# Kernel optimization log

Measured on AMD Instinct MI355X. Metric: run time of the kernel, lower is better.

The kernel has to match this reference:

```python
import jax, jax.numpy as jnp
import numpy as np

EMBED = 1024
HEADS = 16
HEAD_DIM = EMBED // HEADS


def setup_inputs() -> dict:
    key = jax.random.key(0)
    ks = jax.random.split(key, 8)
    N, L = 2, 2048
    values = jax.random.normal(ks[0], (N, L, EMBED), dtype=jnp.float32)
    keys_ = jax.random.normal(ks[1], (N, L, EMBED), dtype=jnp.float32)
    query = jax.random.normal(ks[2], (N, L, EMBED), dtype=jnp.float32)
    mask = jnp.ones((N, 1, 1, L), dtype=jnp.int32)
    s = 1.0 / np.sqrt(EMBED)
    W_q = jax.random.normal(ks[3], (EMBED, EMBED), dtype=jnp.float32) * s
    W_k = jax.random.normal(ks[4], (EMBED, EMBED), dtype=jnp.float32) * s
    W_v = jax.random.normal(ks[5], (EMBED, EMBED), dtype=jnp.float32) * s
    W_o = jax.random.normal(ks[6], (EMBED, EMBED), dtype=jnp.float32) * s
    b_o = jax.random.normal(ks[7], (EMBED,), dtype=jnp.float32) * 0.01
    return {"values": values, "keys": keys_, "query": query, "mask": mask,
            "W_q": W_q, "W_k": W_k, "W_v": W_v, "W_o": W_o, "b_o": b_o}


def reference(values, keys, query, mask, W_q, W_k, W_v, W_o, b_o):
    N, Lq, _ = query.shape
    Lk = keys.shape[1]
    # projections (torch Linear: x @ W.T); reshape to (N, H, L, Dh)
    q = (query @ W_q.T).reshape(N, Lq, HEADS, HEAD_DIM).transpose(0, 2, 1, 3)
    k = (keys @ W_k.T).reshape(N, Lk, HEADS, HEAD_DIM).transpose(0, 2, 1, 3)
    v = (values @ W_v.T).reshape(N, Lk, HEADS, HEAD_DIM).transpose(0, 2, 1, 3)
    energy = jnp.einsum('bhqd,bhkd->bhqk', q, k) / jnp.sqrt(jnp.float32(HEAD_DIM))
    energy = jnp.where(mask == 0, jnp.float32(-1e20), energy)
    attn = jax.nn.softmax(energy, axis=-1)
    out = jnp.einsum('bhqk,bhkd->bhqd', attn, v)
    out = out.transpose(0, 2, 1, 3).reshape(N, Lq, EMBED)
    return out @ W_o.T + b_o
```

## Files before the change

### kernel.cpp

```cpp
#include <hip/hip_runtime.h>
#include <cstddef>
#include <cstdint>

#define SEQ    2048
#define NBATCH 2

typedef unsigned short u16;
typedef unsigned int   u32;
typedef __attribute__((ext_vector_type(8))) short bf16x8;
typedef __attribute__((ext_vector_type(4))) float f32x4;

#if __has_builtin(__builtin_amdgcn_exp2f)
#define EXP2F(x) __builtin_amdgcn_exp2f(x)
#else
#define EXP2F(x) exp2f(x)
#endif

#define GLL16(g, l) __builtin_amdgcn_global_load_lds( \
    (const __attribute__((address_space(1))) void*)(g), \
    (__attribute__((address_space(3))) void*)(l), 16, 0, 0)

__device__ __forceinline__ u32 fbits(float x) { union { float f; u32 u; } c; c.f = x; return c.u; }
__device__ __forceinline__ u16 f2bf(float x) { return (u16)((fbits(x) + 0x8000u) >> 16); }
__device__ __forceinline__ u32 pack2bf(float lo, float hi) {
    return __builtin_amdgcn_perm(fbits(hi) + 0x8000u, fbits(lo) + 0x8000u, 0x07060302u);
}

__global__ __launch_bounds__(256)
void cast_w(const float* __restrict__ wq, const float* __restrict__ wk,
            const float* __restrict__ wv, const float* __restrict__ wo,
            u16* __restrict__ owq, u16* __restrict__ owk,
            u16* __restrict__ owv, u16* __restrict__ owo)
{
    const int w = blockIdx.x >> 10, xi = blockIdx.x & 1023;
    const float* s; u16* d;
    if (w == 0)      { s = wq; d = owq; }
    else if (w == 1) { s = wk; d = owk; }
    else if (w == 2) { s = wv; d = owv; }
    else             { s = wo; d = owo; }
    const int i = xi * 256 + threadIdx.x;
    float4 vv = ((const float4*)s)[i];
    uint2 r; r.x = pack2bf(vv.x, vv.y); r.y = pack2bf(vv.z, vv.w);
    ((uint2*)d)[i] = r;
}

__device__ __forceinline__
void gemm_body_f32A(const float* __restrict__ X, const u16* __restrict__ W,
                    void* __restrict__ Yv, const int layout)
{
    __shared__ u16 smem[128 * 72 + 128 * 64];
    u16* As = smem;
    u16* Bs = smem + 128 * 72;

    const int tid  = threadIdx.x;
    const int wave = tid >> 6;
    const int lane = tid & 63;
    const int lm   = lane & 15;
    const int quad = lane >> 4;
    const int m0 = blockIdx.x * 128;
    const int n0 = blockIdx.y * 128;
    const int wr = (wave & 1) * 64;
    const int wc = (wave >> 1) * 64;

    const int srow = tid >> 1;
    const int scol = (tid & 1) * 32;
    const float* xg = X + (size_t)(m0 + srow) * 1024 + scol;
    const int brow = wave * 32 + (lane >> 3);
    const int bcol = (lane & 7) * 8;
    const u16* wg = W + (size_t)(n0 + brow) * 1024 + bcol;

    float4 pa[8];
    #pragma unroll
    for (int p = 0; p < 8; ++p) pa[p] = ((const float4*)xg)[p];

    f32x4 acc[4][4] = {};

    for (int k0 = 0; k0 < 1024; k0 += 64) {
        __syncthreads();
        #pragma unroll
        for (int p = 0; p < 4; ++p) {
            const float4 a = pa[2 * p], b = pa[2 * p + 1];
            union { u32 w[4]; bf16x8 v; } u;
            u.w[0] = pack2bf(a.x, a.y); u.w[1] = pack2bf(a.z, a.w);
            u.w[2] = pack2bf(b.x, b.y); u.w[3] = pack2bf(b.z, b.w);
            *(bf16x8*)&As[srow * 72 + scol + p * 8] = u.v;
            GLL16(wg + k0 + p * 8 * 1024, &Bs[(wave * 32 + p * 8) * 64]);
        }
        __syncthreads();
        if (k0 + 64 < 1024) {
            #pragma unroll
            for (int p = 0; p < 8; ++p)
                pa[p] = ((const float4*)(xg + k0 + 64))[p];
        }
        #pragma unroll
        for (int kk = 0; kk < 64; kk += 32) {
            bf16x8 af[4], bf[4];
            #pragma unroll
            for (int t = 0; t < 4; ++t) {
                af[t] = *(const bf16x8*)&As[(wr + t * 16 + lm) * 72 + kk + quad * 8];
                bf[t] = *(const bf16x8*)&Bs[(wc + t * 16 + lm) * 64 + kk + quad * 8];
            }
            #pragma unroll
            for (int i = 0; i < 4; ++i)
                #pragma unroll
                for (int j = 0; j < 4; ++j)
                    acc[i][j] = __builtin_amdgcn_mfma_f32_16x16x32_bf16(af[i], bf[j], acc[i][j], 0, 0, 0);
        }
    }

    if (layout == 0) {
        u16* Y = (u16*)Yv;
        #pragma unroll
        for (int i = 0; i < 4; ++i)
            #pragma unroll
            for (int j = 0; j < 4; ++j) {
                const int C = n0 + wc + j * 16 + lm;
                #pragma unroll
                for (int r = 0; r < 4; ++r) {
                    const int R = m0 + wr + i * 16 + quad * 4 + r;
                    Y[(size_t)R * 1024 + C] = f2bf(acc[i][j][r]);
                }
            }
    } else {
        __syncthreads();
        u16* T = smem;
        #pragma unroll
        for (int i = 0; i < 4; ++i)
            #pragma unroll
            for (int j = 0; j < 4; ++j) {
                const int col = wc + j * 16 + lm;
                const int row = wr + i * 16 + quad * 4;
                uint2 v;
                v.x = pack2bf(acc[i][j][0], acc[i][j][1]);
                v.y = pack2bf(acc[i][j][2], acc[i][j][3]);
                *(uint2*)&T[col * 132 + row] = v;
            }
        __syncthreads();
        const int dp = tid >> 1, half = (tid & 1) * 64;
        const int nn = m0 >> 11, l0 = m0 & 2047;
        const int C = n0 + dp, h = C >> 6, d = C & 63;
        u16* Y = (u16*)Yv;
        const size_t base = (((size_t)nn * 16 + h) * 64 + d) * SEQ + l0 + half;
        #pragma unroll
        for (int p = 0; p < 8; ++p) {
            bf16x8 v = *(const bf16x8*)&T[dp * 132 + half + p * 8];
            *(bf16x8*)(Y + base + p * 8) = v;
        }
    }
}

__global__ __launch_bounds__(256, 3)
void gemm_qkv(const float* __restrict__ q, const float* __restrict__ k, const float* __restrict__ v,
              const u16* __restrict__ wq, const u16* __restrict__ wk, const u16* __restrict__ wv,
              u16* __restrict__ qb, u16* __restrict__ kb, u16* __restrict__ vt)
{
    if (blockIdx.z == 0)      gemm_body_f32A(q, wq, qb, 0);
    else if (blockIdx.z == 1) gemm_body_f32A(k, wk, kb, 0);
    else                      gemm_body_f32A(v, wv, vt, 2);
}

__global__ __launch_bounds__(256, 2)
void gemm_out64(const u16* __restrict__ X, const u16* __restrict__ W,
                float* __restrict__ Y, const float* __restrict__ bias)
{
    __shared__ u16 As[128 * 64];
    __shared__ u16 Bs[64 * 64];

    const int tid  = threadIdx.x;
    const int wave = tid >> 6;
    const int lane = tid & 63;
    const int lm   = lane & 15;
    const int quad = lane >> 4;
    const int m0 = blockIdx.x * 128;
    const int n0 = blockIdx.y * 64;
    const int wr = (wave & 1) * 64;
    const int wc = (wave >> 1) * 32;

    const int sr8 = lane >> 3, sc8 = (lane & 7) * 8;
    const u16* xg = X + (size_t)(m0 + wave * 32 + sr8) * 1024 + sc8;
    const u16* wg = W + (size_t)(n0 + wave * 16 + sr8) * 1024 + sc8;

    f32x4 acc[4][2] = {};

    for (int k0 = 0; k0 < 1024; k0 += 64) {
        __syncthreads();
        #pragma unroll
        for (int p = 0; p < 4; ++p)
            GLL16(xg + k0 + p * 8 * 1024, &As[(wave * 32 + p * 8) * 64]);
        #pragma unroll
        for (int p = 0; p < 2; ++p)
            GLL16(wg + k0 + p * 8 * 1024, &Bs[(wave * 16 + p * 8) * 64]);
        __syncthreads();
        #pragma unroll
        for (int kk = 0; kk < 64; kk += 32) {
            bf16x8 af[4], bf[2];
            #pragma unroll
            for (int t = 0; t < 4; ++t)
                af[t] = *(const bf16x8*)&As[(wr + t * 16 + lm) * 64 + kk + quad * 8];
            #pragma unroll
            for (int j = 0; j < 2; ++j)
                bf[j] = *(const bf16x8*)&Bs[(wc + j * 16 + lm) * 64 + kk + quad * 8];
            #pragma unroll
            for (int i = 0; i < 4; ++i)
                #pragma unroll
                for (int j = 0; j < 2; ++j)
                    acc[i][j] = __builtin_amdgcn_mfma_f32_16x16x32_bf16(af[i], bf[j], acc[i][j], 0, 0, 0);
        }
    }

    #pragma unroll
    for (int i = 0; i < 4; ++i)
        #pragma unroll
        for (int j = 0; j < 2; ++j) {
            const int C = n0 + wc + j * 16 + lm;
            const float bv = bias[C];
            #pragma unroll
            for (int r = 0; r < 4; ++r) {
                const int R = m0 + wr + i * 16 + quad * 4 + r;
                Y[(size_t)R * 1024 + C] = acc[i][j][r] + bv;
            }
        }
}

__global__ __launch_bounds__(256, 2)
void flash_attn_bf16(const u16* __restrict__ Qb, const u16* __restrict__ Kb,
                     const u16* __restrict__ VT, const int* __restrict__ mask,
                     u16* __restrict__ O)
{
    __shared__ u16 Ks[128 * 72];
    __shared__ u16 Vts[64 * 136];
    __shared__ u16 Ps[4][32 * 72];

    const int tid  = threadIdx.x;
    const int wave = tid >> 6;
    const int lane = tid & 63;
    const int lm   = lane & 15;
    const int quad = lane >> 4;

    const int wid = blockIdx.x;
    const int idx = wid >> 3;
    const int hn  = (wid & 7) + 8 * (idx & 3);
    const int h   = hn & 15, n = hn >> 4;
    const int wq  = (idx >> 2) * 128 + wave * 32;

    const u16* Qh = Qb + ((size_t)n * SEQ) * 1024 + h * 64;
    const u16* Kh = Kb + ((size_t)n * SEQ) * 1024 + h * 64;
    const u16* Vh = VT + (((size_t)n * 16 + h) * 64) * SEQ;
    const int* mk = mask + (size_t)n * SEQ;
    u16* Pw = &Ps[wave][0];

    bf16x8 qf[2][2];
    #pragma unroll
    for (int qt = 0; qt < 2; ++qt)
        #pragma unroll
        for (int s = 0; s < 2; ++s)
            qf[qt][s] = *(const bf16x8*)(Qh + (size_t)(wq + qt * 16 + lm) * 1024 + s * 32 + quad * 8);

    f32x4 o_acc[2][4] = {};
    float l_i[2] = {};

    const int kr = tid >> 1, kc = (tid & 1) * 32;
    const int vr = tid >> 2, vc = (tid & 3) * 32;

    bf16x8 ka[4], va[4];
    #pragma unroll
    for (int p = 0; p < 4; ++p) {
        ka[p] = *(const bf16x8*)(Kh + (size_t)kr * 1024 + kc + p * 8);
        va[p] = *(const bf16x8*)(Vh + (size_t)vr * SEQ + vc + p * 8);
    }

    const float cs = 0.125f * 1.44269504f;

    for (int c0 = 0; c0 < SEQ; c0 += 128) {
        __syncthreads();
        #pragma unroll
        for (int p = 0; p < 4; ++p) {
            *(bf16x8*)&Ks[kr * 72 + kc + p * 8]   = ka[p];
            *(bf16x8*)&Vts[vr * 136 + vc + p * 8] = va[p];
        }
        __syncthreads();

        if (c0 + 128 < SEQ) {
            #pragma unroll
            for (int p = 0; p < 4; ++p) {
                ka[p] = *(const bf16x8*)(Kh + (size_t)(c0 + 128 + kr) * 1024 + kc + p * 8);
                va[p] = *(const bf16x8*)(Vh + (size_t)vr * SEQ + c0 + 128 + vc + p * 8);
            }
        }

        int4 mkv[8];
        #pragma unroll
        for (int kt = 0; kt < 8; ++kt)
            mkv[kt] = *(const int4*)(mk + c0 + kt * 16 + quad * 4);

        f32x4 st[8][2] = {};
        #pragma unroll
        for (int kt = 0; kt < 8; ++kt) {
            bf16x8 kf0 = *(const bf16x8*)&Ks[(kt * 16 + lm) * 72 + quad * 8];
            bf16x8 kf1 = *(const bf16x8*)&Ks[(kt * 16 + lm) * 72 + 32 + quad * 8];
            #pragma unroll
            for (int qt = 0; qt < 2; ++qt) {
                st[kt][qt] = __builtin_amdgcn_mfma_f32_16x16x32_bf16(kf0, qf[qt][0], st[kt][qt], 0, 0, 0);
                st[kt][qt] = __builtin_amdgcn_mfma_f32_16x16x32_bf16(kf1, qf[qt][1], st[kt][qt], 0, 0, 0);
            }
        }

        #pragma unroll
        for (int half = 0; half < 2; ++half) {
            #pragma unroll
            for (int ktl = 0; ktl < 4; ++ktl) {
                const int kt = half * 4 + ktl;
                const int4 mv = mkv[kt];
                const int mm[4] = {mv.x, mv.y, mv.z, mv.w};
                #pragma unroll
                for (int qt = 0; qt < 2; ++qt) {
                    float e[4];
                    #pragma unroll
                    for (int r = 0; r < 4; ++r) {
                        float v = EXP2F(st[kt][qt][r] * cs);
                        v = mm[r] ? v : 0.0f;
                        e[r] = v;
                        l_i[qt] += v;
                    }
                    uint2 w;
                    w.x = pack2bf(e[0], e[1]);
                    w.y = pack2bf(e[2], e[3]);
                    *(uint2*)&Pw[(qt * 16 + lm) * 72 + ktl * 16 + quad * 4] = w;
                }
            }
            #pragma unroll
            for (int ksl = 0; ksl < 2; ++ksl) {
                bf16x8 pf[2];
                #pragma unroll
                for (int qt = 0; qt < 2; ++qt)
                    pf[qt] = *(const bf16x8*)&Pw[(qt * 16 + lm) * 72 + ksl * 32 + quad * 8];
                #pragma unroll
                for (int dt = 0; dt < 4; ++dt) {
                    bf16x8 vf = *(const bf16x8*)&Vts[(dt * 16 + lm) * 136 + half * 64 + ksl * 32 + quad * 8];
                    #pragma unroll
                    for (int qt = 0; qt < 2; ++qt)
                        o_acc[qt][dt] = __builtin_amdgcn_mfma_f32_16x16x32_bf16(pf[qt], vf, o_acc[qt][dt], 0, 0, 0);
                }
            }
        }
    }

    float linv[2][4];
    #pragma unroll
    for (int qt = 0; qt < 2; ++qt) {
        float v = l_i[qt];
        v += __shfl_xor(v, 16);
        v += __shfl_xor(v, 32);
        #pragma unroll
        for (int r = 0; r < 4; ++r)
            linv[qt][r] = 1.0f / __shfl(v, quad * 4 + r);
    }
    #pragma unroll
    for (int qt = 0; qt < 2; ++qt)
        #pragma unroll
        for (int dt = 0; dt < 4; ++dt)
            #pragma unroll
            for (int r = 0; r < 4; ++r) {
                const int ql = wq + qt * 16 + quad * 4 + r;
                const int col = h * 64 + dt * 16 + lm;
                O[((size_t)n * SEQ + ql) * 1024 + col] = f2bf(o_acc[qt][dt][r] * linv[qt][r]);
            }
}

extern "C" void kernel_launch(void* const* d_in, const int* in_sizes, int n_in,
                              void* d_out, int out_size, void* d_ws, size_t ws_size,
                              hipStream_t stream)
{
    const float* values = (const float*)d_in[0];
    const float* keys   = (const float*)d_in[1];
    const float* query  = (const float*)d_in[2];
    const int*   mask   = (const int*)d_in[3];
    const float* W_q    = (const float*)d_in[4];
    const float* W_k    = (const float*)d_in[5];
    const float* W_v    = (const float*)d_in[6];
    const float* W_o    = (const float*)d_in[7];
    const float* b_o    = (const float*)d_in[8];

    const size_t NTOK = (size_t)NBATCH * SEQ * 1024;
    const size_t WSZ  = 1024 * 1024;
    u16* p = (u16*)d_ws;
    u16* qb    = p; p += NTOK;
    u16* kb    = p; p += NTOK;
    u16* vt    = p; p += NTOK;
    u16* attnb = p; p += NTOK;
    u16* wqb   = p; p += WSZ;
    u16* wkb   = p; p += WSZ;
    u16* wvb   = p; p += WSZ;
    u16* wob   = p; p += WSZ;

    cast_w<<<4096, 256, 0, stream>>>(W_q, W_k, W_v, W_o, wqb, wkb, wvb, wob);

    gemm_qkv<<<dim3(32, 8, 3), 256, 0, stream>>>(query, keys, values,
                                                 wqb, wkb, wvb, qb, kb, vt);

    flash_attn_bf16<<<512, 256, 0, stream>>>(qb, kb, vt, mask, attnb);

    gemm_out64<<<dim3(32, 16), 256, 0, stream>>>(attnb, wob, (float*)d_out, b_o);
}
```

Before: 246.2 us.

## Pre-cast activations to bf16 and double-buffer the output GEMM

Result: faster. 232.8 us (-5.5%).

```diff
diff --git a/kernel.cpp b/kernel.cpp
--- a/kernel.cpp
+++ b/kernel.cpp
@@ -27,30 +27,37 @@
 }
 
 __global__ __launch_bounds__(256)
-void cast_w(const float* __restrict__ wq, const float* __restrict__ wk,
-            const float* __restrict__ wv, const float* __restrict__ wo,
-            u16* __restrict__ owq, u16* __restrict__ owk,
-            u16* __restrict__ owv, u16* __restrict__ owo)
-{
-    const int w = blockIdx.x >> 10, xi = blockIdx.x & 1023;
-    const float* s; u16* d;
-    if (w == 0)      { s = wq; d = owq; }
-    else if (w == 1) { s = wk; d = owk; }
-    else if (w == 2) { s = wv; d = owv; }
-    else             { s = wo; d = owo; }
-    const int i = xi * 256 + threadIdx.x;
+void cast_all(const float* __restrict__ q, const float* __restrict__ k, const float* __restrict__ v,
+              const float* __restrict__ wq, const float* __restrict__ wk,
+              const float* __restrict__ wv, const float* __restrict__ wo,
+              u16* __restrict__ oq, u16* __restrict__ ok, u16* __restrict__ ov,
+              u16* __restrict__ owq, u16* __restrict__ owk, u16* __restrict__ owv,
+              u16* __restrict__ owo)
+{
+    const float* s; u16* d; int i;
+    if (blockIdx.y == 0)      { s = q; d = oq; i = blockIdx.x * 256 + threadIdx.x; }
+    else if (blockIdx.y == 1) { s = k; d = ok; i = blockIdx.x * 256 + threadIdx.x; }
+    else if (blockIdx.y == 2) { s = v; d = ov; i = blockIdx.x * 256 + threadIdx.x; }
+    else {
+        const int w = blockIdx.x >> 10, xi = blockIdx.x & 1023;
+        if (w == 0)      { s = wq; d = owq; }
+        else if (w == 1) { s = wk; d = owk; }
+        else if (w == 2) { s = wv; d = owv; }
+        else             { s = wo; d = owo; }
+        i = xi * 256 + threadIdx.x;
+    }
     float4 vv = ((const float4*)s)[i];
     uint2 r; r.x = pack2bf(vv.x, vv.y); r.y = pack2bf(vv.z, vv.w);
     ((uint2*)d)[i] = r;
 }
 
 __device__ __forceinline__
-void gemm_body_f32A(const float* __restrict__ X, const u16* __restrict__ W,
-                    void* __restrict__ Yv, const int layout)
-{
-    __shared__ u16 smem[128 * 72 + 128 * 64];
+void gemm_body(const u16* __restrict__ X, const u16* __restrict__ W,
+               void* __restrict__ Yv, const int layout)
+{
+    __shared__ u16 smem[16896];
     u16* As = smem;
-    u16* Bs = smem + 128 * 72;
+    u16* Bs = smem + 8192;
 
     const int tid  = threadIdx.x;
     const int wave = tid >> 6;
@@ -62,16 +69,10 @@
     const int wr = (wave & 1) * 64;
     const int wc = (wave >> 1) * 64;
 
-    const int srow = tid >> 1;
-    const int scol = (tid & 1) * 32;
-    const float* xg = X + (size_t)(m0 + srow) * 1024 + scol;
-    const int brow = wave * 32 + (lane >> 3);
-    const int bcol = (lane & 7) * 8;
-    const u16* wg = W + (size_t)(n0 + brow) * 1024 + bcol;
-
-    float4 pa[8];
-    #pragma unroll
-    for (int p = 0; p < 8; ++p) pa[p] = ((const float4*)xg)[p];
+    const int srow = wave * 32 + (lane >> 3);
+    const int scol = (lane & 7) * 8;
+    const u16* xg = X + (size_t)(m0 + srow) * 1024 + scol;
+    const u16* wg = W + (size_t)(n0 + srow) * 1024 + scol;
 
     f32x4 acc[4][4] = {};
 
@@ -79,25 +80,16 @@
         __syncthreads();
         #pragma unroll
         for (int p = 0; p < 4; ++p) {
-            const float4 a = pa[2 * p], b = pa[2 * p + 1];
-            union { u32 w[4]; bf16x8 v; } u;
-            u.w[0] = pack2bf(a.x, a.y); u.w[1] = pack2bf(a.z, a.w);
-            u.w[2] = pack2bf(b.x, b.y); u.w[3] = pack2bf(b.z, b.w);
-            *(bf16x8*)&As[srow * 72 + scol + p * 8] = u.v;
+            GLL16(xg + k0 + p * 8 * 1024, &As[(wave * 32 + p * 8) * 64]);
             GLL16(wg + k0 + p * 8 * 1024, &Bs[(wave * 32 + p * 8) * 64]);
         }
         __syncthreads();
-        if (k0 + 64 < 1024) {
-            #pragma unroll
-            for (int p = 0; p < 8; ++p)
-                pa[p] = ((const float4*)(xg + k0 + 64))[p];
-        }
         #pragma unroll
         for (int kk = 0; kk < 64; kk += 32) {
             bf16x8 af[4], bf[4];
             #pragma unroll
             for (int t = 0; t < 4; ++t) {
-                af[t] = *(const bf16x8*)&As[(wr + t * 16 + lm) * 72 + kk + quad * 8];
+                af[t] = *(const bf16x8*)&As[(wr + t * 16 + lm) * 64 + kk + quad * 8];
                 bf[t] = *(const bf16x8*)&Bs[(wc + t * 16 + lm) * 64 + kk + quad * 8];
             }
             #pragma unroll
@@ -150,21 +142,21 @@
 }
 
 __global__ __launch_bounds__(256, 3)
-void gemm_qkv(const float* __restrict__ q, const float* __restrict__ k, const float* __restrict__ v,
+void gemm_qkv(const u16* __restrict__ xq, const u16* __restrict__ xk, const u16* __restrict__ xv,
               const u16* __restrict__ wq, const u16* __restrict__ wk, const u16* __restrict__ wv,
               u16* __restrict__ qb, u16* __restrict__ kb, u16* __restrict__ vt)
 {
-    if (blockIdx.z == 0)      gemm_body_f32A(q, wq, qb, 0);
-    else if (blockIdx.z == 1) gemm_body_f32A(k, wk, kb, 0);
-    else                      gemm_body_f32A(v, wv, vt, 2);
+    if (blockIdx.z == 0)      gemm_body(xq, wq, qb, 0);
+    else if (blockIdx.z == 1) gemm_body(xk, wk, kb, 0);
+    else                      gemm_body(xv, wv, vt, 2);
 }
 
 __global__ __launch_bounds__(256, 2)
 void gemm_out64(const u16* __restrict__ X, const u16* __restrict__ W,
                 float* __restrict__ Y, const float* __restrict__ bias)
 {
-    __shared__ u16 As[128 * 64];
-    __shared__ u16 Bs[64 * 64];
+    __shared__ u16 As[2][128 * 64];
+    __shared__ u16 Bs[2][64 * 64];
 
     const int tid  = threadIdx.x;
     const int wave = tid >> 6;
@@ -180,32 +172,44 @@
     const u16* xg = X + (size_t)(m0 + wave * 32 + sr8) * 1024 + sc8;
     const u16* wg = W + (size_t)(n0 + wave * 16 + sr8) * 1024 + sc8;
 
+    #pragma unroll
+    for (int p = 0; p < 4; ++p)
+        GLL16(xg + p * 8 * 1024, &As[0][(wave * 32 + p * 8) * 64]);
+    #pragma unroll
+    for (int p = 0; p < 2; ++p)
+        GLL16(wg + p * 8 * 1024, &Bs[0][(wave * 16 + p * 8) * 64]);
+
     f32x4 acc[4][2] = {};
-
-    for (int k0 = 0; k0 < 1024; k0 += 64) {
-        __syncthreads();
-        #pragma unroll
-        for (int p = 0; p < 4; ++p)
-            GLL16(xg + k0 + p * 8 * 1024, &As[(wave * 32 + p * 8) * 64]);
-        #pragma unroll
-        for (int p = 0; p < 2; ++p)
-            GLL16(wg + k0 + p * 8 * 1024, &Bs[(wave * 16 + p * 8) * 64]);
-        __syncthreads();
+    __syncthreads();
+
+    #pragma unroll
+    for (int it = 0; it < 16; ++it) {
+        const int cur = it & 1;
+        if (it + 1 < 16) {
+            const int kn = (it + 1) * 64;
+            #pragma unroll
+            for (int p = 0; p < 4; ++p)
+                GLL16(xg + kn + p * 8 * 1024, &As[cur ^ 1][(wave * 32 + p * 8) * 64]);
+            #pragma unroll
+            for (int p = 0; p < 2; ++p)
+                GLL16(wg + kn + p * 8 * 1024, &Bs[cur ^ 1][(wave * 16 + p * 8) * 64]);
+        }
         #pragma unroll
         for (int kk = 0; kk < 64; kk += 32) {
             bf16x8 af[4], bf[2];
             #pragma unroll
             for (int t = 0; t < 4; ++t)
-                af[t] = *(const bf16x8*)&As[(wr + t * 16 + lm) * 64 + kk + quad * 8];
+                af[t] = *(const bf16x8*)&As[cur][(wr + t * 16 + lm) * 64 + kk + quad * 8];
             #pragma unroll
             for (int j = 0; j < 2; ++j)
-                bf[j] = *(const bf16x8*)&Bs[(wc + j * 16 + lm) * 64 + kk + quad * 8];
+                bf[j] = *(const bf16x8*)&Bs[cur][(wc + j * 16 + lm) * 64 + kk + quad * 8];
             #pragma unroll
             for (int i = 0; i < 4; ++i)
                 #pragma unroll
                 for (int j = 0; j < 2; ++j)
                     acc[i][j] = __builtin_amdgcn_mfma_f32_16x16x32_bf16(af[i], bf[j], acc[i][j], 0, 0, 0);
         }
+        __syncthreads();
     }
 
     #pragma unroll
@@ -387,16 +391,20 @@
     u16* qb    = p; p += NTOK;
     u16* kb    = p; p += NTOK;
     u16* vt    = p; p += NTOK;
+    u16* xq    = p; p += NTOK;
+    u16* xk    = p; p += NTOK;
+    u16* xv    = p; p += NTOK;
     u16* attnb = p; p += NTOK;
     u16* wqb   = p; p += WSZ;
     u16* wkb   = p; p += WSZ;
     u16* wvb   = p; p += WSZ;
     u16* wob   = p; p += WSZ;
 
-    cast_w<<<4096, 256, 0, stream>>>(W_q, W_k, W_v, W_o, wqb, wkb, wvb, wob);
-
-    gemm_qkv<<<dim3(32, 8, 3), 256, 0, stream>>>(query, keys, values,
-                                                 wqb, wkb, wvb, qb, kb, vt);
+    cast_all<<<dim3(4096, 4), 256, 0, stream>>>(query, keys, values,
+                                                W_q, W_k, W_v, W_o,
+                                                xq, xk, xv, wqb, wkb, wvb, wob);
+
+    gemm_qkv<<<dim3(32, 8, 3), 256, 0, stream>>>(xq, xk, xv, wqb, wkb, wvb, qb, kb, vt);
 
     flash_attn_bf16<<<512, 256, 0, stream>>>(qb, kb, vt, mask, attnb);
 
```
